# Performance work log

Measured on AMD Instinct MI355X. Metric: run time of the kernel, lower is better.

Reference implementation:

```python
import jax, jax.numpy as jnp
import numpy as np

# dims: batch B, frames F_, spatial tokens N, heads H, head dim D, model dim DIM
B, F_, N, H, D, DIM = 1, 16, 1024, 8, 64, 512


def setup_inputs() -> dict:
    key = jax.random.key(0)
    k1, k2, k3, k4 = jax.random.split(key, 4)
    x = jax.random.normal(k1, (B, F_ * N, DIM), dtype=jnp.float32)
    W_qkv = jax.random.normal(k2, (DIM, 3 * H * D), dtype=jnp.float32) * 0.02
    W_out = jax.random.normal(k3, (H * D, DIM), dtype=jnp.float32) * 0.02
    mask = jax.random.randint(k4, (1, 1, N), 0, 2, dtype=jnp.int32)
    return {"x": x, "W_qkv": W_qkv, "W_out": W_out, "mask": mask, "diag": 1}


def reference(x, W_qkv, W_out, mask, diag):
    scale = D ** -0.5
    qkv = x @ W_qkv                      # [B, F*N, 3*H*D]
    q, k, v = jnp.split(qkv, 3, axis=-1)

    def split_heads(t):                  # 'b n (h d) -> (b h) n d'
        return t.reshape(B, F_ * N, H, D).transpose(0, 2, 1, 3).reshape(B * H, F_ * N, D)

    q, k, v = map(split_heads, (q, k, v))
    q = q * scale

    def axial(t):                        # '(b h) (f n) d -> (b h f) n d'
        return t.reshape(B * H * F_, N, D)

    q, k, v = map(axial, (q, k, v))

    sim = jnp.einsum('bid,bjd->bij', q, k)        # [(B*H*F), N, N]
    neg = -jnp.finfo(sim.dtype).max
    if diag:
        sim = jnp.where(jnp.eye(N, dtype=bool)[None], neg, sim)
    sim = jnp.where(mask == 0, neg, sim)           # padding mask broadcast
    attn = jax.nn.softmax(sim, axis=-1)
    out = jnp.einsum('bij,bjd->bid', attn, v)      # [(B*H*F), N, D]

    # '(b h f) n d -> (b h) (f n) d' then '(b h) n d -> b n (h d)'
    out = out.reshape(B, H, F_ * N, D).transpose(0, 2, 1, 3).reshape(B, F_ * N, H * D)
    return out @ W_out
```

## Files before the change

kernel.cpp:

```cpp
#include <hip/hip_runtime.h>
#include <stdint.h>

typedef __bf16 bf16;
typedef __bf16 bf16x8 __attribute__((ext_vector_type(8)));
typedef float f32x4 __attribute__((ext_vector_type(4)));

__device__ __forceinline__ void gload_lds16(const void* g, void* l) {
    __builtin_amdgcn_global_load_lds((const __attribute__((address_space(1))) void*)g,
                                     (__attribute__((address_space(3))) void*)l, 16, 0, 0);
}

__device__ __forceinline__ float fast_exp2(float x) { return __builtin_amdgcn_exp2f(x); }

__global__ __launch_bounds__(256) void k_prep(const float* __restrict__ x, bf16* __restrict__ xb,
                                              const float* __restrict__ Wqkv, bf16* __restrict__ WqT,
                                              const float* __restrict__ Wout, bf16* __restrict__ WoT,
                                              const int* __restrict__ mask, int* __restrict__ idxU,
                                              int* __restrict__ cpos, int* __restrict__ meta) {
    __shared__ float t[32][33];
    __shared__ int lsum[256];
    int b = blockIdx.x, tid = threadIdx.x;
    if (b < 4096) {
        int i = b * 256 + tid;
        const f32x4* p = (const f32x4*)(x + (size_t)i * 8);
        f32x4 a = p[0], c = p[1];
        bf16x8 o;
        o[0] = (bf16)a[0]; o[1] = (bf16)a[1]; o[2] = (bf16)a[2]; o[3] = (bf16)a[3];
        o[4] = (bf16)c[0]; o[5] = (bf16)c[1]; o[6] = (bf16)c[2]; o[7] = (bf16)c[3];
        *(bf16x8*)(xb + (size_t)i * 8) = o;
    } else if (b < 4096 + 768 + 256) {
        const float* W; bf16* WT; int C, bb;
        if (b < 4096 + 768) { W = Wqkv; WT = WqT; C = 1536; bb = b - 4096; }
        else                { W = Wout; WT = WoT; C = 512;  bb = b - 4864; }
        int nblk = C / 32;
        int n0 = (bb % nblk) * 32, k0 = (bb / nblk) * 32;
        int tx = tid & 31, ty = tid >> 5;
        for (int i = 0; i < 32; i += 8) t[ty + i][tx] = W[(size_t)(k0 + ty + i) * C + n0 + tx];
        __syncthreads();
        for (int i = 0; i < 32; i += 8) WT[(size_t)(n0 + ty + i) * 512 + k0 + tx] = (bf16)t[tx][ty + i];
    } else {
        int m[4], s = 0;
#pragma unroll
        for (int e = 0; e < 4; e++) { m[e] = mask[4 * tid + e]; s += m[e]; }
        lsum[tid] = s;
        __syncthreads();
        for (int off = 1; off < 256; off <<= 1) {
            int v = (tid >= off) ? lsum[tid - off] : 0;
            __syncthreads();
            lsum[tid] += v;
            __syncthreads();
        }
        int run = lsum[tid] - s;
#pragma unroll
        for (int e = 0; e < 4; e++) {
            if (m[e]) { idxU[run] = 4 * tid + e; cpos[4 * tid + e] = run; run++; }
            else cpos[4 * tid + e] = -1;
        }
        int nU = lsum[255];
        for (int i = nU + tid; i < 1024; i += 256) idxU[i] = 0;
        if (tid == 255) { meta[0] = nU; meta[1] = (nU + 63) >> 6; }
    }
}

__global__ __launch_bounds__(256) void k_qkv(const bf16* __restrict__ Xb, const bf16* __restrict__ WT,
                                             bf16* __restrict__ Qb, bf16* __restrict__ Kb, bf16* __restrict__ Vb) {
    __shared__ char As[2][8192], Bs[2][8192];
    int tid = threadIdx.x, l = tid & 63, w = tid >> 6;
    int wy = w >> 1, wx = w & 1;
    int id = blockIdx.x;
    int wg = (id & 7) * 192 + (id >> 3);
    int bm = (wg / 12) * 128, bn = (wg % 12) * 128;
    int lr = l & 15, kg = l >> 4;

    int subr = l >> 2, chk = l & 3;
    int R0 = w * 32 + subr,      m0 = (R0 >> 1) & 3, c0 = chk ^ m0;
    int R1 = w * 32 + 16 + subr, m1 = (R1 >> 1) & 3, c1 = chk ^ m1;

    f32x4 acc[4][4] = {};

    gload_lds16((const char*)Xb + ((size_t)(bm + R0) * 512) * 2 + c0 * 16, As[0] + w * 2048 + l * 16);
    gload_lds16((const char*)Xb + ((size_t)(bm + R1) * 512) * 2 + c1 * 16, As[0] + w * 2048 + 1024 + l * 16);
    gload_lds16((const char*)WT + ((size_t)(bn + R0) * 512) * 2 + c0 * 16, Bs[0] + w * 2048 + l * 16);
    gload_lds16((const char*)WT + ((size_t)(bn + R1) * 512) * 2 + c1 * 16, Bs[0] + w * 2048 + 1024 + l * 16);
    __syncthreads();

    for (int t = 0; t < 16; t++) {
        int cur = t & 1;
        if (t < 15) {
            int k1 = (t + 1) * 32;
            gload_lds16((const char*)Xb + ((size_t)(bm + R0) * 512 + k1) * 2 + c0 * 16, As[cur ^ 1] + w * 2048 + l * 16);
            gload_lds16((const char*)Xb + ((size_t)(bm + R1) * 512 + k1) * 2 + c1 * 16, As[cur ^ 1] + w * 2048 + 1024 + l * 16);
            gload_lds16((const char*)WT + ((size_t)(bn + R0) * 512 + k1) * 2 + c0 * 16, Bs[cur ^ 1] + w * 2048 + l * 16);
            gload_lds16((const char*)WT + ((size_t)(bn + R1) * 512 + k1) * 2 + c1 * 16, Bs[cur ^ 1] + w * 2048 + 1024 + l * 16);
        }

        bf16x8 af[4], bfr[4];
#pragma unroll
        for (int mt = 0; mt < 4; mt++) {
            int r = wy * 64 + mt * 16 + lr;
            af[mt] = *(const bf16x8*)(As[cur] + r * 64 + ((kg ^ ((r >> 1) & 3)) << 4));
        }
#pragma unroll
        for (int nt = 0; nt < 4; nt++) {
            int r = wx * 64 + nt * 16 + lr;
            bfr[nt] = *(const bf16x8*)(Bs[cur] + r * 64 + ((kg ^ ((r >> 1) & 3)) << 4));
        }
#pragma unroll
        for (int mt = 0; mt < 4; mt++)
#pragma unroll
            for (int nt = 0; nt < 4; nt++)
                acc[mt][nt] = __builtin_amdgcn_mfma_f32_16x16x32_bf16(af[mt], bfr[nt], acc[mt][nt], 0, 0, 0);

        __syncthreads();
    }

#pragma unroll
    for (int mt = 0; mt < 4; mt++) {
#pragma unroll
        for (int nt = 0; nt < 4; nt++) {
            int c = bn + wx * 64 + nt * 16 + lr;
            int which = c >> 9, hd = c & 511, h = hd >> 6, d = hd & 63;
            float qs = (which == 0) ? 0.18033688f : 1.0f;
            bf16* base = (which == 0) ? Qb : (which == 1) ? Kb : Vb;
#pragma unroll
            for (int j = 0; j < 4; j++) {
                int m = bm + wy * 64 + mt * 16 + kg * 4 + j;
                int f = m >> 10, nn = m & 1023;
                base[((size_t)(h * 16 + f) * 1024 + nn) * 64 + d] = (bf16)(acc[mt][nt][j] * qs);
            }
        }
    }
}

__global__ __launch_bounds__(256) void k_vtg(const bf16* __restrict__ V, bf16* __restrict__ Vtc,
                                             const int* __restrict__ idxU, const int* __restrict__ meta) {
    __shared__ bf16 t[64][80];
    int bp = blockIdx.y, c0 = blockIdx.x * 64;
    int nU = meta[0], nUp = meta[1] << 6;
    if (c0 >= nUp) return;
    int tid = threadIdx.x;
    int nl = tid >> 2, dc = (tid & 3) * 16;
    int c = c0 + nl;
    bf16x8 a0 = {}, a1 = {};
    if (c < nU) {
        int row = idxU[c];
        const bf16* src = V + ((size_t)bp * 1024 + row) * 64 + dc;
        a0 = *(const bf16x8*)src;
        a1 = *(const bf16x8*)(src + 8);
    }
    *(bf16x8*)&t[nl][dc] = a0;
    *(bf16x8*)&t[nl][dc + 8] = a1;
    __syncthreads();
    int dl = tid >> 2, nc = (tid & 3) * 16;
    bf16x8 o0, o1;
#pragma unroll
    for (int i = 0; i < 8; i++) o0[i] = t[nc + i][dl];
#pragma unroll
    for (int i = 0; i < 8; i++) o1[i] = t[nc + 8 + i][dl];
    bf16* dst = Vtc + ((size_t)bp * 64 + dl) * 1024 + c0 + nc;
    *(bf16x8*)dst = o0;
    *(bf16x8*)(dst + 8) = o1;
}

__global__ __launch_bounds__(512) void k_attn(const bf16* __restrict__ Qb, const bf16* __restrict__ Kb,
                                              const bf16* __restrict__ Vtc, bf16* __restrict__ AO,
                                              const int* __restrict__ cpos, const int* __restrict__ idxU,
                                              const int* __restrict__ meta, const int* __restrict__ diagp) {
    __shared__ char Ks[8192], Vs[8192], Ps[16384];
    int tid = threadIdx.x, l = tid & 63, w = tid >> 6;
    int id = blockIdx.x;
    int wg = (id & 7) * 128 + (id >> 3);
    int qt = wg & 7, bp = wg >> 3;
    int lr = l & 15, kg = l >> 4;
    int diag = diagp[0];
    int nU = meta[0], nT = meta[1];

    int nq = qt * 128 + w * 16 + lr;
    const char* Qrow = (const char*)Qb + ((size_t)bp * 1024 + nq) * 128;
    bf16x8 qf0 = *(const bf16x8*)(Qrow + kg * 16);
    bf16x8 qf1 = *(const bf16x8*)(Qrow + 64 + kg * 16);

    int cq[4];
#pragma unroll
    for (int j = 0; j < 4; j++) {
        int qg = qt * 128 + w * 16 + kg * 4 + j;
        cq[j] = diag ? cpos[qg] : -1;
    }
    int cqmax = cq[0];
#pragma unroll
    for (int j = 1; j < 4; j++) cqmax = (cq[j] > cqmax) ? cq[j] : cqmax;
    int cqmin = cq[0];
#pragma unroll
    for (int j = 1; j < 4; j++) cqmin = (cq[j] < cqmin) ? cq[j] : cqmin;
    int dtile_lo = cqmin >> 6, dtile_hi = cqmax >> 6;

    const char* Kbb = (const char*)Kb + (size_t)bp * 1024 * 128;
    const char* Vbase = (const char*)Vtc + (size_t)bp * 64 * 2048;

    int rs = tid >> 3;
    int cs = (tid & 7) ^ (rs & 7);

    f32x4 o[4] = {};
    f32x4 psum = {0.f, 0.f, 0.f, 0.f};

    bf16x8 kreg = *(const bf16x8*)(Kbb + (size_t)idxU[rs] * 128 + cs * 16);
    bf16x8 vreg = *(const bf16x8*)(Vbase + (size_t)rs * 2048 + cs * 16);

    for (int kt = 0; kt < nT; kt++) {
        __syncthreads();
        *(bf16x8*)(Ks + tid * 16) = kreg;
        *(bf16x8*)(Vs + tid * 16) = vreg;
        if (kt + 1 < nT) {
            kreg = *(const bf16x8*)(Kbb + (size_t)idxU[(kt + 1) * 64 + rs] * 128 + cs * 16);
            vreg = *(const bf16x8*)(Vbase + (size_t)rs * 2048 + (kt + 1) * 128 + cs * 16);
        }
        __syncthreads();

        f32x4 s[4] = {};
        __builtin_amdgcn_s_setprio(1);
#pragma unroll
        for (int nt = 0; nt < 4; nt++) {
            int r = nt * 16 + lr;
            bf16x8 kf0 = *(const bf16x8*)(Ks + r * 128 + ((kg ^ (r & 7)) << 4));
            bf16x8 kf1 = *(const bf16x8*)(Ks + r * 128 + (((4 + kg) ^ (r & 7)) << 4));
            s[nt] = __builtin_amdgcn_mfma_f32_16x16x32_bf16(qf0, kf0, s[nt], 0, 0, 0);
            s[nt] = __builtin_amdgcn_mfma_f32_16x16x32_bf16(qf1, kf1, s[nt], 0, 0, 0);
        }
        __builtin_amdgcn_s_setprio(0);

#pragma unroll
        for (int nt = 0; nt < 4; nt++)
#pragma unroll
            for (int j = 0; j < 4; j++) s[nt][j] = fast_exp2(s[nt][j]);

        if (kt == nT - 1) {
            float mf0 = (kt * 64 + lr < nU) ? 1.f : 0.f;
            float mf1 = (kt * 64 + 16 + lr < nU) ? 1.f : 0.f;
            float mf2 = (kt * 64 + 32 + lr < nU) ? 1.f : 0.f;
            float mf3 = (kt * 64 + 48 + lr < nU) ? 1.f : 0.f;
#pragma unroll
            for (int j = 0; j < 4; j++) {
                s[0][j] *= mf0; s[1][j] *= mf1; s[2][j] *= mf2; s[3][j] *= mf3;
            }
        }
        if (kt >= dtile_lo && kt <= dtile_hi) {
#pragma unroll
            for (int nt = 0; nt < 4; nt++) {
                int c = kt * 64 + nt * 16 + lr;
#pragma unroll
                for (int j = 0; j < 4; j++)
                    if (c == cq[j]) s[nt][j] = 0.f;
            }
        }
#pragma unroll
        for (int j = 0; j < 4; j++) psum[j] += (s[0][j] + s[1][j]) + (s[2][j] + s[3][j]);

#pragma unroll
        for (int nt = 0; nt < 4; nt++)
#pragma unroll
            for (int j = 0; j < 4; j++) {
                int rq = w * 16 + kg * 4 + j;
                int byte = (rq * 128 + (nt * 16 + lr) * 2) ^ ((rq & 7) << 4);
                *(bf16*)(Ps + byte) = (bf16)s[nt][j];
            }

        int rp = w * 16 + lr;
        bf16x8 pf0 = *(const bf16x8*)(Ps + rp * 128 + ((kg ^ (rp & 7)) << 4));
        bf16x8 pf1 = *(const bf16x8*)(Ps + rp * 128 + (((4 + kg) ^ (rp & 7)) << 4));
        __builtin_amdgcn_s_setprio(1);
#pragma unroll
        for (int dt = 0; dt < 4; dt++) {
            int rd = dt * 16 + lr;
            bf16x8 vf0 = *(const bf16x8*)(Vs + rd * 128 + ((kg ^ (rd & 7)) << 4));
            bf16x8 vf1 = *(const bf16x8*)(Vs + rd * 128 + (((4 + kg) ^ (rd & 7)) << 4));
            o[dt] = __builtin_amdgcn_mfma_f32_16x16x32_bf16(pf0, vf0, o[dt], 0, 0, 0);
            o[dt] = __builtin_amdgcn_mfma_f32_16x16x32_bf16(pf1, vf1, o[dt], 0, 0, 0);
        }
        __builtin_amdgcn_s_setprio(0);
    }

#pragma unroll
    for (int off = 1; off < 16; off <<= 1)
#pragma unroll
        for (int j = 0; j < 4; j++) psum[j] += __shfl_xor(psum[j], off, 64);
    float inv[4];
#pragma unroll
    for (int j = 0; j < 4; j++) inv[j] = 1.0f / psum[j];

    int f = bp & 15, h = bp >> 4;
#pragma unroll
    for (int dt = 0; dt < 4; dt++)
#pragma unroll
        for (int j = 0; j < 4; j++) {
            int n = qt * 128 + w * 16 + kg * 4 + j;
            size_t m = (size_t)f * 1024 + n;
            AO[m * 512 + h * 64 + dt * 16 + lr] = (bf16)(o[dt][j] * inv[j]);
        }
}

__global__ __launch_bounds__(256) void k_out(const bf16* __restrict__ Ab, const bf16* __restrict__ WT,
                                             float* __restrict__ out) {
    __shared__ char As[2][8192], Bs[2][8192];
    int tid = threadIdx.x, l = tid & 63, w = tid >> 6;
    int wy = w >> 1, wx = w & 1;
    int id = blockIdx.x;
    int wg = (id & 7) * 64 + (id >> 3);
    int bm = (wg / 4) * 128, bn = (wg % 4) * 128;
    int lr = l & 15, kg = l >> 4;

    int subr = l >> 2, chk = l & 3;
    int R0 = w * 32 + subr,      m0 = (R0 >> 1) & 3, c0 = chk ^ m0;
    int R1 = w * 32 + 16 + subr, m1 = (R1 >> 1) & 3, c1 = chk ^ m1;

    f32x4 acc[4][4] = {};

    gload_lds16((const char*)Ab + ((size_t)(bm + R0) * 512) * 2 + c0 * 16, As[0] + w * 2048 + l * 16);
    gload_lds16((const char*)Ab + ((size_t)(bm + R1) * 512) * 2 + c1 * 16, As[0] + w * 2048 + 1024 + l * 16);
    gload_lds16((const char*)WT + ((size_t)(bn + R0) * 512) * 2 + c0 * 16, Bs[0] + w * 2048 + l * 16);
    gload_lds16((const char*)WT + ((size_t)(bn + R1) * 512) * 2 + c1 * 16, Bs[0] + w * 2048 + 1024 + l * 16);
    __syncthreads();

    for (int t = 0; t < 16; t++) {
        int cur = t & 1;
        if (t < 15) {
            int k1 = (t + 1) * 32;
            gload_lds16((const char*)Ab + ((size_t)(bm + R0) * 512 + k1) * 2 + c0 * 16, As[cur ^ 1] + w * 2048 + l * 16);
            gload_lds16((const char*)Ab + ((size_t)(bm + R1) * 512 + k1) * 2 + c1 * 16, As[cur ^ 1] + w * 2048 + 1024 + l * 16);
            gload_lds16((const char*)WT + ((size_t)(bn + R0) * 512 + k1) * 2 + c0 * 16, Bs[cur ^ 1] + w * 2048 + l * 16);
            gload_lds16((const char*)WT + ((size_t)(bn + R1) * 512 + k1) * 2 + c1 * 16, Bs[cur ^ 1] + w * 2048 + 1024 + l * 16);
        }

        bf16x8 af[4], bfr[4];
#pragma unroll
        for (int mt = 0; mt < 4; mt++) {
            int r = wy * 64 + mt * 16 + lr;
            af[mt] = *(const bf16x8*)(As[cur] + r * 64 + ((kg ^ ((r >> 1) & 3)) << 4));
        }
#pragma unroll
        for (int nt = 0; nt < 4; nt++) {
            int r = wx * 64 + nt * 16 + lr;
            bfr[nt] = *(const bf16x8*)(Bs[cur] + r * 64 + ((kg ^ ((r >> 1) & 3)) << 4));
        }
#pragma unroll
        for (int mt = 0; mt < 4; mt++)
#pragma unroll
            for (int nt = 0; nt < 4; nt++)
                acc[mt][nt] = __builtin_amdgcn_mfma_f32_16x16x32_bf16(af[mt], bfr[nt], acc[mt][nt], 0, 0, 0);

        __syncthreads();
    }

#pragma unroll
    for (int mt = 0; mt < 4; mt++)
#pragma unroll
        for (int nt = 0; nt < 4; nt++) {
            int c = bn + wx * 64 + nt * 16 + lr;
#pragma unroll
            for (int j = 0; j < 4; j++) {
                int m = bm + wy * 64 + mt * 16 + kg * 4 + j;
                out[(size_t)m * 512 + c] = acc[mt][nt][j];
            }
        }
}

extern "C" void kernel_launch(void* const* d_in, const int* in_sizes, int n_in,
                              void* d_out, int out_size, void* d_ws, size_t ws_size,
                              hipStream_t stream) {
    const float* x    = (const float*)d_in[0];
    const float* Wqkv = (const float*)d_in[1];
    const float* Wout = (const float*)d_in[2];
    const int*   mask = (const int*)d_in[3];
    const int*   diag = (const int*)d_in[4];
    float* out = (float*)d_out;
    char* ws = (char*)d_ws;

    bf16* Xb  = (bf16*)(ws);
    bf16* Vtc = (bf16*)(ws);
    bf16* WqT = (bf16*)(ws + ((size_t)16 << 20));
    bf16* WoT = (bf16*)(ws + ((size_t)18 << 20));
    int*  idxU = (int*)(ws + ((size_t)18 << 20) + (1 << 19));
    int*  cpos = (int*)(ws + ((size_t)18 << 20) + (1 << 19) + 4096);
    int*  meta = (int*)(ws + ((size_t)18 << 20) + (1 << 19) + 8192);
    bf16* Qb  = (bf16*)(ws + ((size_t)19 << 20));
    bf16* Kb  = (bf16*)(ws + ((size_t)35 << 20));
    bf16* Vb  = (bf16*)(ws + ((size_t)51 << 20));
    bf16* AO  = (bf16*)(ws + ((size_t)67 << 20));

    hipLaunchKernelGGL(k_prep, dim3(4096 + 768 + 256 + 1), dim3(256), 0, stream,
                       x, Xb, Wqkv, WqT, Wout, WoT, mask, idxU, cpos, meta);
    hipLaunchKernelGGL(k_qkv, dim3(1536), dim3(256), 0, stream, Xb, WqT, Qb, Kb, Vb);
    hipLaunchKernelGGL(k_vtg, dim3(16, 128), dim3(256), 0, stream, Vb, Vtc, idxU, meta);
    hipLaunchKernelGGL(k_attn, dim3(1024), dim3(512), 0, stream, Qb, Kb, Vtc, AO, cpos, idxU, meta, diag);
    hipLaunchKernelGGL(k_out, dim3(512), dim3(256), 0, stream, AO, WoT, out);
}
```

Measured before the change: 109.5 us.

## Fuse fp32-to-bf16 conversion of x into QKV GEMM operand loading

Removes the separate x-to-bf16 conversion pass in the prep kernel and instead loads fp32 x directly in the QKV GEMM, converting to bf16 in registers before writing to LDS. The GEMM pipeline changes from async global-to-LDS double buffering to register prefetch with a single LDS buffer and two barriers per k-step. This saves a 32 MB fp32 read plus a 16 MB bf16 write/read round trip. In exchange, each QKV block rereads x at twice the byte width, once per N-tile, and loses the direct-to-LDS async copies.

```diff
diff --git a/kernel.cpp b/kernel.cpp
--- a/kernel.cpp
+++ b/kernel.cpp
@@ -12,26 +12,17 @@
 
 __device__ __forceinline__ float fast_exp2(float x) { return __builtin_amdgcn_exp2f(x); }
 
-__global__ __launch_bounds__(256) void k_prep(const float* __restrict__ x, bf16* __restrict__ xb,
-                                              const float* __restrict__ Wqkv, bf16* __restrict__ WqT,
+__global__ __launch_bounds__(256) void k_prep(const float* __restrict__ Wqkv, bf16* __restrict__ WqT,
                                               const float* __restrict__ Wout, bf16* __restrict__ WoT,
                                               const int* __restrict__ mask, int* __restrict__ idxU,
                                               int* __restrict__ cpos, int* __restrict__ meta) {
     __shared__ float t[32][33];
     __shared__ int lsum[256];
     int b = blockIdx.x, tid = threadIdx.x;
-    if (b < 4096) {
-        int i = b * 256 + tid;
-        const f32x4* p = (const f32x4*)(x + (size_t)i * 8);
-        f32x4 a = p[0], c = p[1];
-        bf16x8 o;
-        o[0] = (bf16)a[0]; o[1] = (bf16)a[1]; o[2] = (bf16)a[2]; o[3] = (bf16)a[3];
-        o[4] = (bf16)c[0]; o[5] = (bf16)c[1]; o[6] = (bf16)c[2]; o[7] = (bf16)c[3];
-        *(bf16x8*)(xb + (size_t)i * 8) = o;
-    } else if (b < 4096 + 768 + 256) {
+    if (b < 768 + 256) {
         const float* W; bf16* WT; int C, bb;
-        if (b < 4096 + 768) { W = Wqkv; WT = WqT; C = 1536; bb = b - 4096; }
-        else                { W = Wout; WT = WoT; C = 512;  bb = b - 4864; }
+        if (b < 768) { W = Wqkv; WT = WqT; C = 1536; bb = b; }
+        else         { W = Wout; WT = WoT; C = 512;  bb = b - 768; }
         int nblk = C / 32;
         int n0 = (bb % nblk) * 32, k0 = (bb / nblk) * 32;
         int tx = tid & 31, ty = tid >> 5;
@@ -62,9 +53,9 @@
     }
 }
 
-__global__ __launch_bounds__(256) void k_qkv(const bf16* __restrict__ Xb, const bf16* __restrict__ WT,
+__global__ __launch_bounds__(256) void k_qkv(const float* __restrict__ X, const bf16* __restrict__ WT,
                                              bf16* __restrict__ Qb, bf16* __restrict__ Kb, bf16* __restrict__ Vb) {
-    __shared__ char As[2][8192], Bs[2][8192];
+    __shared__ char As[8192], Bs[8192];
     int tid = threadIdx.x, l = tid & 63, w = tid >> 6;
     int wy = w >> 1, wx = w & 1;
     int id = blockIdx.x;
@@ -73,45 +64,56 @@
     int lr = l & 15, kg = l >> 4;
 
     int subr = l >> 2, chk = l & 3;
-    int R0 = w * 32 + subr,      m0 = (R0 >> 1) & 3, c0 = chk ^ m0;
-    int R1 = w * 32 + 16 + subr, m1 = (R1 >> 1) & 3, c1 = chk ^ m1;
+    int R0 = w * 32 + subr,      c0 = chk ^ ((R0 >> 1) & 3);
+    int R1 = R0 + 16,            c1 = chk ^ ((R1 >> 1) & 3);
+
+    const float* xA0 = X + (size_t)(bm + R0) * 512 + c0 * 8;
+    const float* xA1 = X + (size_t)(bm + R1) * 512 + c1 * 8;
+    const bf16*  wB0 = WT + (size_t)(bn + R0) * 512 + c0 * 8;
+    const bf16*  wB1 = WT + (size_t)(bn + R1) * 512 + c1 * 8;
+
+    f32x4 a0lo = *(const f32x4*)(xA0), a0hi = *(const f32x4*)(xA0 + 4);
+    f32x4 a1lo = *(const f32x4*)(xA1), a1hi = *(const f32x4*)(xA1 + 4);
+    bf16x8 b0 = *(const bf16x8*)(wB0), b1 = *(const bf16x8*)(wB1);
 
     f32x4 acc[4][4] = {};
 
-    gload_lds16((const char*)Xb + ((size_t)(bm + R0) * 512) * 2 + c0 * 16, As[0] + w * 2048 + l * 16);
-    gload_lds16((const char*)Xb + ((size_t)(bm + R1) * 512) * 2 + c1 * 16, As[0] + w * 2048 + 1024 + l * 16);
-    gload_lds16((const char*)WT + ((size_t)(bn + R0) * 512) * 2 + c0 * 16, Bs[0] + w * 2048 + l * 16);
-    gload_lds16((const char*)WT + ((size_t)(bn + R1) * 512) * 2 + c1 * 16, Bs[0] + w * 2048 + 1024 + l * 16);
-    __syncthreads();
-
     for (int t = 0; t < 16; t++) {
-        int cur = t & 1;
+        __syncthreads();
+        bf16x8 a0, a1;
+#pragma unroll
+        for (int i = 0; i < 4; i++) {
+            a0[i] = (bf16)a0lo[i]; a0[4 + i] = (bf16)a0hi[i];
+            a1[i] = (bf16)a1lo[i]; a1[4 + i] = (bf16)a1hi[i];
+        }
+        *(bf16x8*)(As + w * 2048 + l * 16) = a0;
+        *(bf16x8*)(As + w * 2048 + 1024 + l * 16) = a1;
+        *(bf16x8*)(Bs + w * 2048 + l * 16) = b0;
+        *(bf16x8*)(Bs + w * 2048 + 1024 + l * 16) = b1;
         if (t < 15) {
             int k1 = (t + 1) * 32;
-            gload_lds16((const char*)Xb + ((size_t)(bm + R0) * 512 + k1) * 2 + c0 * 16, As[cur ^ 1] + w * 2048 + l * 16);
-            gload_lds16((const char*)Xb + ((size_t)(bm + R1) * 512 + k1) * 2 + c1 * 16, As[cur ^ 1] + w * 2048 + 1024 + l * 16);
-            gload_lds16((const char*)WT + ((size_t)(bn + R0) * 512 + k1) * 2 + c0 * 16, Bs[cur ^ 1] + w * 2048 + l * 16);
-            gload_lds16((const char*)WT + ((size_t)(bn + R1) * 512 + k1) * 2 + c1 * 16, Bs[cur ^ 1] + w * 2048 + 1024 + l * 16);
-        }
+            a0lo = *(const f32x4*)(xA0 + k1); a0hi = *(const f32x4*)(xA0 + k1 + 4);
+            a1lo = *(const f32x4*)(xA1 + k1); a1hi = *(const f32x4*)(xA1 + k1 + 4);
+            b0 = *(const bf16x8*)(wB0 + k1); b1 = *(const bf16x8*)(wB1 + k1);
+        }
+        __syncthreads();
 
         bf16x8 af[4], bfr[4];
 #pragma unroll
         for (int mt = 0; mt < 4; mt++) {
             int r = wy * 64 + mt * 16 + lr;
-            af[mt] = *(const bf16x8*)(As[cur] + r * 64 + ((kg ^ ((r >> 1) & 3)) << 4));
+            af[mt] = *(const bf16x8*)(As + r * 64 + ((kg ^ ((r >> 1) & 3)) << 4));
         }
 #pragma unroll
         for (int nt = 0; nt < 4; nt++) {
             int r = wx * 64 + nt * 16 + lr;
-            bfr[nt] = *(const bf16x8*)(Bs[cur] + r * 64 + ((kg ^ ((r >> 1) & 3)) << 4));
+            bfr[nt] = *(const bf16x8*)(Bs + r * 64 + ((kg ^ ((r >> 1) & 3)) << 4));
         }
 #pragma unroll
         for (int mt = 0; mt < 4; mt++)
 #pragma unroll
             for (int nt = 0; nt < 4; nt++)
                 acc[mt][nt] = __builtin_amdgcn_mfma_f32_16x16x32_bf16(af[mt], bfr[nt], acc[mt][nt], 0, 0, 0);
-
-        __syncthreads();
     }
 
 #pragma unroll
@@ -374,7 +376,6 @@
     float* out = (float*)d_out;
     char* ws = (char*)d_ws;
 
-    bf16* Xb  = (bf16*)(ws);
     bf16* Vtc = (bf16*)(ws);
     bf16* WqT = (bf16*)(ws + ((size_t)16 << 20));
     bf16* WoT = (bf16*)(ws + ((size_t)18 << 20));
@@ -386,9 +387,9 @@
     bf16* Vb  = (bf16*)(ws + ((size_t)51 << 20));
     bf16* AO  = (bf16*)(ws + ((size_t)67 << 20));
 
-    hipLaunchKernelGGL(k_prep, dim3(4096 + 768 + 256 + 1), dim3(256), 0, stream,
-                       x, Xb, Wqkv, WqT, Wout, WoT, mask, idxU, cpos, meta);
-    hipLaunchKernelGGL(k_qkv, dim3(1536), dim3(256), 0, stream, Xb, WqT, Qb, Kb, Vb);
+    hipLaunchKernelGGL(k_prep, dim3(768 + 256 + 1), dim3(256), 0, stream,
+                       Wqkv, WqT, Wout, WoT, mask, idxU, cpos, meta);
+    hipLaunchKernelGGL(k_qkv, dim3(1536), dim3(256), 0, stream, x, WqT, Qb, Kb, Vb);
     hipLaunchKernelGGL(k_vtg, dim3(16, 128), dim3(256), 0, stream, Vb, Vtc, idxU, meta);
     hipLaunchKernelGGL(k_attn, dim3(1024), dim3(512), 0, stream, Qb, Kb, Vtc, AO, cpos, idxU, meta, diag);
     hipLaunchKernelGGL(k_out, dim3(512), dim3(256), 0, stream, AO, WoT, out);
```

After: 111.5 us. About the same (+1.8%).

## Triple-buffer LDS in QKV and output GEMMs with one barrier per k-step

Applied to the files above, without the earlier changes.

Both projection GEMMs move from double-buffered to triple-buffered LDS staging. Each k-step now waits with an explicit vmcnt(4) and a single barrier, then computes on the current buffer while issuing loads two stages ahead, with sched_barriers to hold the instruction order. The goal is to hide global-to-LDS latency better and drop the second barrier per iteration. In exchange, LDS use per block grows from 32KB to 48KB, which can lower occupancy, and correctness now rests on the hand-counted vmcnt values.

```diff
diff --git a/kernel.cpp b/kernel.cpp
--- a/kernel.cpp
+++ b/kernel.cpp
@@ -64,7 +64,7 @@
 
 __global__ __launch_bounds__(256) void k_qkv(const bf16* __restrict__ Xb, const bf16* __restrict__ WT,
                                              bf16* __restrict__ Qb, bf16* __restrict__ Kb, bf16* __restrict__ Vb) {
-    __shared__ char As[2][8192], Bs[2][8192];
+    __shared__ char As[3][8192], Bs[3][8192];
     int tid = threadIdx.x, l = tid & 63, w = tid >> 6;
     int wy = w >> 1, wx = w & 1;
     int id = blockIdx.x;
@@ -73,46 +73,63 @@
     int lr = l & 15, kg = l >> 4;
 
     int subr = l >> 2, chk = l & 3;
-    int R0 = w * 32 + subr,      m0 = (R0 >> 1) & 3, c0 = chk ^ m0;
-    int R1 = w * 32 + 16 + subr, m1 = (R1 >> 1) & 3, c1 = chk ^ m1;
+    int R0 = w * 32 + subr,      c0 = chk ^ ((R0 >> 1) & 3);
+    int R1 = w * 32 + 16 + subr, c1 = chk ^ ((R1 >> 1) & 3);
+
+    const char* xA0 = (const char*)Xb + ((size_t)(bm + R0) * 512) * 2 + c0 * 16;
+    const char* xA1 = (const char*)Xb + ((size_t)(bm + R1) * 512) * 2 + c1 * 16;
+    const char* wB0 = (const char*)WT + ((size_t)(bn + R0) * 512) * 2 + c0 * 16;
+    const char* wB1 = (const char*)WT + ((size_t)(bn + R1) * 512) * 2 + c1 * 16;
 
     f32x4 acc[4][4] = {};
 
-    gload_lds16((const char*)Xb + ((size_t)(bm + R0) * 512) * 2 + c0 * 16, As[0] + w * 2048 + l * 16);
-    gload_lds16((const char*)Xb + ((size_t)(bm + R1) * 512) * 2 + c1 * 16, As[0] + w * 2048 + 1024 + l * 16);
-    gload_lds16((const char*)WT + ((size_t)(bn + R0) * 512) * 2 + c0 * 16, Bs[0] + w * 2048 + l * 16);
-    gload_lds16((const char*)WT + ((size_t)(bn + R1) * 512) * 2 + c1 * 16, Bs[0] + w * 2048 + 1024 + l * 16);
-    __syncthreads();
-
-    for (int t = 0; t < 16; t++) {
-        int cur = t & 1;
-        if (t < 15) {
-            int k1 = (t + 1) * 32;
-            gload_lds16((const char*)Xb + ((size_t)(bm + R0) * 512 + k1) * 2 + c0 * 16, As[cur ^ 1] + w * 2048 + l * 16);
-            gload_lds16((const char*)Xb + ((size_t)(bm + R1) * 512 + k1) * 2 + c1 * 16, As[cur ^ 1] + w * 2048 + 1024 + l * 16);
-            gload_lds16((const char*)WT + ((size_t)(bn + R0) * 512 + k1) * 2 + c0 * 16, Bs[cur ^ 1] + w * 2048 + l * 16);
-            gload_lds16((const char*)WT + ((size_t)(bn + R1) * 512 + k1) * 2 + c1 * 16, Bs[cur ^ 1] + w * 2048 + 1024 + l * 16);
-        }
-
-        bf16x8 af[4], bfr[4];
-#pragma unroll
-        for (int mt = 0; mt < 4; mt++) {
-            int r = wy * 64 + mt * 16 + lr;
-            af[mt] = *(const bf16x8*)(As[cur] + r * 64 + ((kg ^ ((r >> 1) & 3)) << 4));
-        }
-#pragma unroll
-        for (int nt = 0; nt < 4; nt++) {
-            int r = wx * 64 + nt * 16 + lr;
-            bfr[nt] = *(const bf16x8*)(Bs[cur] + r * 64 + ((kg ^ ((r >> 1) & 3)) << 4));
-        }
-#pragma unroll
-        for (int mt = 0; mt < 4; mt++)
-#pragma unroll
-            for (int nt = 0; nt < 4; nt++)
-                acc[mt][nt] = __builtin_amdgcn_mfma_f32_16x16x32_bf16(af[mt], bfr[nt], acc[mt][nt], 0, 0, 0);
-
-        __syncthreads();
-    }
+#define QKV_STAGE(T, BUF)                                                   \
+    do {                                                                    \
+        int k0b = (T) * 64;                                                 \
+        gload_lds16(xA0 + k0b, As[BUF] + w * 2048 + l * 16);                \
+        gload_lds16(xA1 + k0b, As[BUF] + w * 2048 + 1024 + l * 16);         \
+        gload_lds16(wB0 + k0b, Bs[BUF] + w * 2048 + l * 16);                \
+        gload_lds16(wB1 + k0b, Bs[BUF] + w * 2048 + 1024 + l * 16);         \
+    } while (0)
+
+    QKV_STAGE(0, 0);
+    QKV_STAGE(1, 1);
+
+#define QKV_COMPUTE(CUR)                                                    \
+    do {                                                                    \
+        bf16x8 af[4], bfr[4];                                               \
+        _Pragma("unroll")                                                   \
+        for (int mt = 0; mt < 4; mt++) {                                    \
+            int r = wy * 64 + mt * 16 + lr;                                 \
+            af[mt] = *(const bf16x8*)(As[CUR] + r * 64 + ((kg ^ ((r >> 1) & 3)) << 4)); \
+        }                                                                   \
+        _Pragma("unroll")                                                   \
+        for (int nt = 0; nt < 4; nt++) {                                    \
+            int r = wx * 64 + nt * 16 + lr;                                 \
+            bfr[nt] = *(const bf16x8*)(Bs[CUR] + r * 64 + ((kg ^ ((r >> 1) & 3)) << 4)); \
+        }                                                                   \
+        _Pragma("unroll")                                                   \
+        for (int mt = 0; mt < 4; mt++)                                      \
+            _Pragma("unroll")                                               \
+            for (int nt = 0; nt < 4; nt++)                                  \
+                acc[mt][nt] = __builtin_amdgcn_mfma_f32_16x16x32_bf16(af[mt], bfr[nt], acc[mt][nt], 0, 0, 0); \
+    } while (0)
+
+    for (int t = 0; t < 15; t++) {
+        asm volatile("s_waitcnt vmcnt(4)" ::: "memory");
+        __builtin_amdgcn_s_barrier();
+        __builtin_amdgcn_sched_barrier(0);
+        int cur = t % 3;
+        QKV_COMPUTE(cur);
+        if (t + 2 < 16) QKV_STAGE(t + 2, (t + 2) % 3);
+        __builtin_amdgcn_sched_barrier(0);
+    }
+    asm volatile("s_waitcnt vmcnt(0)" ::: "memory");
+    __builtin_amdgcn_s_barrier();
+    __builtin_amdgcn_sched_barrier(0);
+    QKV_COMPUTE(15 % 3);
+#undef QKV_STAGE
+#undef QKV_COMPUTE
 
 #pragma unroll
     for (int mt = 0; mt < 4; mt++) {
@@ -300,7 +317,7 @@
 
 __global__ __launch_bounds__(256) void k_out(const bf16* __restrict__ Ab, const bf16* __restrict__ WT,
                                              float* __restrict__ out) {
-    __shared__ char As[2][8192], Bs[2][8192];
+    __shared__ char As[3][8192], Bs[3][8192];
     int tid = threadIdx.x, l = tid & 63, w = tid >> 6;
     int wy = w >> 1, wx = w & 1;
     int id = blockIdx.x;
@@ -309,46 +326,63 @@
     int lr = l & 15, kg = l >> 4;
 
     int subr = l >> 2, chk = l & 3;
-    int R0 = w * 32 + subr,      m0 = (R0 >> 1) & 3, c0 = chk ^ m0;
-    int R1 = w * 32 + 16 + subr, m1 = (R1 >> 1) & 3, c1 = chk ^ m1;
+    int R0 = w * 32 + subr,      c0 = chk ^ ((R0 >> 1) & 3);
+    int R1 = w * 32 + 16 + subr, c1 = chk ^ ((R1 >> 1) & 3);
+
+    const char* aA0 = (const char*)Ab + ((size_t)(bm + R0) * 512) * 2 + c0 * 16;
+    const char* aA1 = (const char*)Ab + ((size_t)(bm + R1) * 512) * 2 + c1 * 16;
+    const char* wB0 = (const char*)WT + ((size_t)(bn + R0) * 512) * 2 + c0 * 16;
+    const char* wB1 = (const char*)WT + ((size_t)(bn + R1) * 512) * 2 + c1 * 16;
 
     f32x4 acc[4][4] = {};
 
-    gload_lds16((const char*)Ab + ((size_t)(bm + R0) * 512) * 2 + c0 * 16, As[0] + w * 2048 + l * 16);
-    gload_lds16((const char*)Ab + ((size_t)(bm + R1) * 512) * 2 + c1 * 16, As[0] + w * 2048 + 1024 + l * 16);
-    gload_lds16((const char*)WT + ((size_t)(bn + R0) * 512) * 2 + c0 * 16, Bs[0] + w * 2048 + l * 16);
-    gload_lds16((const char*)WT + ((size_t)(bn + R1) * 512) * 2 + c1 * 16, Bs[0] + w * 2048 + 1024 + l * 16);
-    __syncthreads();
-
-    for (int t = 0; t < 16; t++) {
-        int cur = t & 1;
-        if (t < 15) {
-            int k1 = (t + 1) * 32;
-            gload_lds16((const char*)Ab + ((size_t)(bm + R0) * 512 + k1) * 2 + c0 * 16, As[cur ^ 1] + w * 2048 + l * 16);
-            gload_lds16((const char*)Ab + ((size_t)(bm + R1) * 512 + k1) * 2 + c1 * 16, As[cur ^ 1] + w * 2048 + 1024 + l * 16);
-            gload_lds16((const char*)WT + ((size_t)(bn + R0) * 512 + k1) * 2 + c0 * 16, Bs[cur ^ 1] + w * 2048 + l * 16);
-            gload_lds16((const char*)WT + ((size_t)(bn + R1) * 512 + k1) * 2 + c1 * 16, Bs[cur ^ 1] + w * 2048 + 1024 + l * 16);
-        }
-
-        bf16x8 af[4], bfr[4];
-#pragma unroll
-        for (int mt = 0; mt < 4; mt++) {
-            int r = wy * 64 + mt * 16 + lr;
-            af[mt] = *(const bf16x8*)(As[cur] + r * 64 + ((kg ^ ((r >> 1) & 3)) << 4));
-        }
-#pragma unroll
-        for (int nt = 0; nt < 4; nt++) {
-            int r = wx * 64 + nt * 16 + lr;
-            bfr[nt] = *(const bf16x8*)(Bs[cur] + r * 64 + ((kg ^ ((r >> 1) & 3)) << 4));
-        }
-#pragma unroll
-        for (int mt = 0; mt < 4; mt++)
-#pragma unroll
-            for (int nt = 0; nt < 4; nt++)
-                acc[mt][nt] = __builtin_amdgcn_mfma_f32_16x16x32_bf16(af[mt], bfr[nt], acc[mt][nt], 0, 0, 0);
-
-        __syncthreads();
-    }
+#define OUT_STAGE(T, BUF)                                                   \
+    do {                                                                    \
+        int k0b = (T) * 64;                                                 \
+        gload_lds16(aA0 + k0b, As[BUF] + w * 2048 + l * 16);                \
+        gload_lds16(aA1 + k0b, As[BUF] + w * 2048 + 1024 + l * 16);         \
+        gload_lds16(wB0 + k0b, Bs[BUF] + w * 2048 + l * 16);                \
+        gload_lds16(wB1 + k0b, Bs[BUF] + w * 2048 + 1024 + l * 16);         \
+    } while (0)
+
+    OUT_STAGE(0, 0);
+    OUT_STAGE(1, 1);
+
+#define OUT_COMPUTE(CUR)                                                    \
+    do {                                                                    \
+        bf16x8 af[4], bfr[4];                                               \
+        _Pragma("unroll")                                                   \
+        for (int mt = 0; mt < 4; mt++) {                                    \
+            int r = wy * 64 + mt * 16 + lr;                                 \
+            af[mt] = *(const bf16x8*)(As[CUR] + r * 64 + ((kg ^ ((r >> 1) & 3)) << 4)); \
+        }                                                                   \
+        _Pragma("unroll")                                                   \
+        for (int nt = 0; nt < 4; nt++) {                                    \
+            int r = wx * 64 + nt * 16 + lr;                                 \
+            bfr[nt] = *(const bf16x8*)(Bs[CUR] + r * 64 + ((kg ^ ((r >> 1) & 3)) << 4)); \
+        }                                                                   \
+        _Pragma("unroll")                                                   \
+        for (int mt = 0; mt < 4; mt++)                                      \
+            _Pragma("unroll")                                               \
+            for (int nt = 0; nt < 4; nt++)                                  \
+                acc[mt][nt] = __builtin_amdgcn_mfma_f32_16x16x32_bf16(af[mt], bfr[nt], acc[mt][nt], 0, 0, 0); \
+    } while (0)
+
+    for (int t = 0; t < 15; t++) {
+        asm volatile("s_waitcnt vmcnt(4)" ::: "memory");
+        __builtin_amdgcn_s_barrier();
+        __builtin_amdgcn_sched_barrier(0);
+        int cur = t % 3;
+        OUT_COMPUTE(cur);
+        if (t + 2 < 16) OUT_STAGE(t + 2, (t + 2) % 3);
+        __builtin_amdgcn_sched_barrier(0);
+    }
+    asm volatile("s_waitcnt vmcnt(0)" ::: "memory");
+    __builtin_amdgcn_s_barrier();
+    __builtin_amdgcn_sched_barrier(0);
+    OUT_COMPUTE(15 % 3);
+#undef OUT_STAGE
+#undef OUT_COMPUTE
 
 #pragma unroll
     for (int mt = 0; mt < 4; mt++)
```

New measurement: 108.8 us. Within noise of the previous version (-0.7%).
